# Kernel tuning notes

Measured on AMD Instinct MI355X. Metric: run time of the kernel, lower is better.

Reference implementation:

```python
import jax, jax.numpy as jnp
import numpy as np

B, S, D, H = 2, 2048, 1024, 16
HD = D // H
MASK_VALUE = -1000000.0


def setup_inputs() -> dict:
    key = jax.random.key(0)
    ks = jax.random.split(key, 8)
    scale = 1.0 / np.sqrt(D)
    return {
        "Q": jax.random.normal(ks[0], (B, S, D), jnp.float32),
        "K": jax.random.normal(ks[1], (B, S, D), jnp.float32),
        "V": jax.random.normal(ks[2], (B, S, D), jnp.float32),
        "valid_lens": jax.random.randint(ks[3], (B,), 0, S).astype(jnp.int32),
        "Wq": jax.random.normal(ks[4], (D, D), jnp.float32) * scale,
        "Wk": jax.random.normal(ks[5], (D, D), jnp.float32) * scale,
        "Wv": jax.random.normal(ks[6], (D, D), jnp.float32) * scale,
        "Wo": jax.random.normal(ks[7], (D, D), jnp.float32) * scale,
    }


def _split_heads(x):
    # [B,S,D] -> [B,H,S,HD]
    return x.reshape(B, S, H, HD).transpose(0, 2, 1, 3)


def reference(Q, K, V, valid_lens, Wq, Wk, Wv, Wo):
    q = _split_heads(Q @ Wq)
    k = _split_heads(K @ Wk)
    v = _split_heads(V @ Wv)
    # scores: [B,H,Sq,Sk]
    scores = jnp.einsum("bhqd,bhkd->bhqk", q, k) / jnp.sqrt(jnp.float32(HD))
    # mask key positions >= valid_len (per batch, broadcast over heads/queries)
    key_pos = jnp.arange(S)  # [Sk]
    mask = key_pos[None, None, None, :] < valid_lens[:, None, None, None]
    scores = jnp.where(mask, scores, MASK_VALUE)
    attn = jax.nn.softmax(scores, axis=-1)
    out = jnp.einsum("bhqk,bhkd->bhqd", attn, v)  # [B,H,S,HD]
    out = out.transpose(0, 2, 1, 3).reshape(B, S, D)
    return out @ Wo
```

## Files before the change

### kernel.cpp

```cpp
#include <hip/hip_runtime.h>
#include <stdint.h>

#define B_ 2
#define S_ 2048
#define D_ 1024
#define H_ 16
#define HD_ 64
#define MG_ (B_*S_)
#define MASKV -1000000.0f
#define LP_ 72
#define LO_ 68

typedef __bf16 bf16;
typedef bf16 bf16x8 __attribute__((ext_vector_type(8)));
typedef bf16 bf16x4 __attribute__((ext_vector_type(4)));
typedef float f32x4 __attribute__((ext_vector_type(4)));

#define MFMA(a, b, c) __builtin_amdgcn_mfma_f32_16x16x32_bf16(a, b, c, 0, 0, 0)

__global__ __launch_bounds__(256) void wcast_kernel(const float* __restrict__ W0, const float* __restrict__ W1,
                                                    const float* __restrict__ W2, const float* __restrict__ W3,
                                                    bf16* __restrict__ T) {
  const float* W = blockIdx.z == 0 ? W0 : blockIdx.z == 1 ? W1 : blockIdx.z == 2 ? W2 : W3;
  bf16* Tz = T + (size_t)blockIdx.z * D_ * D_;
  __shared__ float tile[32][33];
  int tx = threadIdx.x & 31, ty = threadIdx.x >> 5;
  int bn = blockIdx.x * 32, bk = blockIdx.y * 32;
#pragma unroll
  for (int i = 0; i < 32; i += 8)
    tile[ty + i][tx] = W[(size_t)(bk + ty + i) * D_ + bn + tx];
  __syncthreads();
#pragma unroll
  for (int i = 0; i < 32; i += 8)
    Tz[(size_t)(bn + ty + i) * D_ + bk + tx] = (bf16)tile[tx][ty + i];
}

__global__ __launch_bounds__(256) void proj_gemm(const float* __restrict__ Qin, const float* __restrict__ Kin,
                                                 const float* __restrict__ Vin, const bf16* __restrict__ WT,
                                                 bf16* __restrict__ qh, bf16* __restrict__ kh,
                                                 bf16* __restrict__ vT) {
  __shared__ alignas(16) bf16 As[128 * 32];
  __shared__ alignas(16) bf16 Bs[128 * 32];
  int mode = blockIdx.z;
  int tid = threadIdx.x, lane = tid & 63, w = tid >> 6;
  int wm = w >> 1, wn = w & 1, ml = lane & 15, quad = lane >> 4;
  int rr = tid >> 3, c4 = (tid & 7) * 4;
  f32x4 acc[4][4] = {};

  if (mode < 2) {
    const float* A = mode ? Kin : Qin;
    const bf16* Bt = WT + (size_t)mode * D_ * D_;
    bf16* dst = mode ? kh : qh;
    float oscale = mode ? 1.0f : 0.125f;
    int m0 = blockIdx.y * 128, n0 = blockIdx.x * 128;
    for (int kk = 0; kk < D_; kk += 32) {
      __syncthreads();
#pragma unroll
      for (int p = 0; p < 4; ++p) {
        float4 v = *(const float4*)&A[(size_t)(m0 + rr + p * 32) * D_ + kk + c4];
        bf16x4 bv; bv[0] = (bf16)v.x; bv[1] = (bf16)v.y; bv[2] = (bf16)v.z; bv[3] = (bf16)v.w;
        *(bf16x4*)&As[(rr + p * 32) * 32 + c4] = bv;
      }
#pragma unroll
      for (int p = 0; p < 2; ++p) {
        int cc = tid + p * 256;
        int nr = cc >> 2, c8 = (cc & 3) * 8;
        *(bf16x8*)&Bs[nr * 32 + c8] = *(const bf16x8*)&Bt[(size_t)(n0 + nr) * D_ + kk + c8];
      }
      __syncthreads();
      bf16x8 af[4], bfr[4];
#pragma unroll
      for (int mt = 0; mt < 4; ++mt) af[mt] = *(bf16x8*)&As[(wm * 64 + mt * 16 + ml) * 32 + quad * 8];
#pragma unroll
      for (int nt = 0; nt < 4; ++nt) bfr[nt] = *(bf16x8*)&Bs[(wn * 64 + nt * 16 + ml) * 32 + quad * 8];
#pragma unroll
      for (int mt = 0; mt < 4; ++mt)
#pragma unroll
        for (int nt = 0; nt < 4; ++nt)
          acc[mt][nt] = MFMA(af[mt], bfr[nt], acc[mt][nt]);
    }
#pragma unroll
    for (int mt = 0; mt < 4; ++mt)
#pragma unroll
      for (int nt = 0; nt < 4; ++nt)
#pragma unroll
        for (int r = 0; r < 4; ++r) {
          int m = m0 + wm * 64 + mt * 16 + quad * 4 + r;
          int n = n0 + wn * 64 + nt * 16 + ml;
          int b = m >> 11, s = m & (S_ - 1), h = n >> 6, hd = n & 63;
          dst[(((size_t)(b * H_ + h)) * S_ + s) * HD_ + hd] = (bf16)(acc[mt][nt][r] * oscale);
        }
  } else {
    const bf16* At = WT + 2ull * D_ * D_;
    int m0 = blockIdx.x * 128;
    int n0 = blockIdx.y * 128;
    for (int kk = 0; kk < D_; kk += 32) {
      __syncthreads();
#pragma unroll
      for (int p = 0; p < 2; ++p) {
        int cc = tid + p * 256;
        int nr = cc >> 2, c8 = (cc & 3) * 8;
        *(bf16x8*)&As[nr * 32 + c8] = *(const bf16x8*)&At[(size_t)(m0 + nr) * D_ + kk + c8];
      }
#pragma unroll
      for (int p = 0; p < 4; ++p) {
        float4 v = *(const float4*)&Vin[(size_t)(n0 + rr + p * 32) * D_ + kk + c4];
        bf16x4 bv; bv[0] = (bf16)v.x; bv[1] = (bf16)v.y; bv[2] = (bf16)v.z; bv[3] = (bf16)v.w;
        *(bf16x4*)&Bs[(rr + p * 32) * 32 + c4] = bv;
      }
      __syncthreads();
      bf16x8 af[4], bfr[4];
#pragma unroll
      for (int mt = 0; mt < 4; ++mt) af[mt] = *(bf16x8*)&As[(wm * 64 + mt * 16 + ml) * 32 + quad * 8];
#pragma unroll
      for (int nt = 0; nt < 4; ++nt) bfr[nt] = *(bf16x8*)&Bs[(wn * 64 + nt * 16 + ml) * 32 + quad * 8];
#pragma unroll
      for (int mt = 0; mt < 4; ++mt)
#pragma unroll
        for (int nt = 0; nt < 4; ++nt)
          acc[mt][nt] = MFMA(af[mt], bfr[nt], acc[mt][nt]);
    }
#pragma unroll
    for (int mt = 0; mt < 4; ++mt)
#pragma unroll
      for (int nt = 0; nt < 4; ++nt)
#pragma unroll
        for (int r = 0; r < 4; ++r) {
          int dcol = m0 + wm * 64 + mt * 16 + quad * 4 + r;
          int n = n0 + wn * 64 + nt * 16 + ml;
          int b = n >> 11, s = n & (S_ - 1), h = dcol >> 6, hd = dcol & 63;
          vT[(((size_t)(b * H_ + h)) * HD_ + hd) * S_ + s] = (bf16)acc[mt][nt][r];
        }
  }
}

__global__ __launch_bounds__(256) void attn_kernel(const bf16* __restrict__ qh, const bf16* __restrict__ kh,
                                                   const bf16* __restrict__ vT, const int* __restrict__ vlen,
                                                   bf16* __restrict__ ctx) {
  __shared__ alignas(16) char ldsraw[35840];
  bf16* Ps = (bf16*)ldsraw;
  float* Om = (float*)ldsraw;
  float* Mv = (float*)(ldsraw + 34816);
  float* Lv = (float*)(ldsraw + 35328);

  int tid = threadIdx.x, lane = tid & 63, w = tid >> 6;
  int ml = lane & 15, quad = lane >> 4;
  int wq = w >> 1, wk = w & 1;
  int bh = blockIdx.y, b = bh >> 4, h = bh & 15;
  int qt = blockIdx.x;
  const bf16* qbase = qh + ((size_t)bh * S_ + qt * 64 + wq * 32) * HD_;
  const bf16* kbase = kh + (size_t)bh * S_ * HD_;
  const bf16* vbase = vT + (size_t)bh * HD_ * S_;
  int valid = vlen[b];
  int nkt = (valid == 0) ? (S_ / 64) : ((valid + 63) >> 6);

  bf16x8 aq[2][2];
#pragma unroll
  for (int mt = 0; mt < 2; ++mt)
#pragma unroll
    for (int half = 0; half < 2; ++half)
      aq[mt][half] = *(const bf16x8*)&qbase[(mt * 16 + ml) * HD_ + half * 32 + quad * 8];

  float m_run[2][4], l_run[2][4];
#pragma unroll
  for (int mt = 0; mt < 2; ++mt)
#pragma unroll
    for (int r = 0; r < 4; ++r) { m_run[mt][r] = -1e30f; l_run[mt][r] = 0.f; }
  f32x4 o[2][4] = {};

  bf16* Pw = Ps + (size_t)w * 32 * LP_;

  for (int kt = wk; kt < nkt; kt += 2) {
    const bf16* kp = kbase + (size_t)kt * 64 * HD_;
    bool tail = (kt * 64 + 64 > valid);
    bf16x8 bk[4][2];
#pragma unroll
    for (int nt = 0; nt < 4; ++nt)
#pragma unroll
      for (int half = 0; half < 2; ++half)
        bk[nt][half] = *(const bf16x8*)&kp[(nt * 16 + ml) * HD_ + half * 32 + quad * 8];

#pragma unroll
    for (int mt = 0; mt < 2; ++mt) {
      f32x4 sc[4];
#pragma unroll
      for (int nt = 0; nt < 4; ++nt) {
        f32x4 c = {};
        c = MFMA(aq[mt][0], bk[nt][0], c);
        c = MFMA(aq[mt][1], bk[nt][1], c);
        sc[nt] = c;
      }
#pragma unroll
      for (int r = 0; r < 4; ++r) {
        float mx = -1e30f;
#pragma unroll
        for (int nt = 0; nt < 4; ++nt) {
          float s = sc[nt][r];
          if (tail) {
            int col = kt * 64 + nt * 16 + ml;
            if (col >= valid) s = MASKV;
          }
          sc[nt][r] = s;
          mx = fmaxf(mx, s);
        }
#pragma unroll
        for (int d = 1; d < 16; d <<= 1) mx = fmaxf(mx, __shfl_xor(mx, d));
        float mnew = fmaxf(m_run[mt][r], mx);
        float ps = 0.f;
#pragma unroll
        for (int nt = 0; nt < 4; ++nt) {
          float p = __expf(sc[nt][r] - mnew);
          sc[nt][r] = p;
          ps += p;
        }
#pragma unroll
        for (int d = 1; d < 16; d <<= 1) ps += __shfl_xor(ps, d);
        float alpha = __expf(m_run[mt][r] - mnew);
        l_run[mt][r] = l_run[mt][r] * alpha + ps;
        m_run[mt][r] = mnew;
#pragma unroll
        for (int ht = 0; ht < 4; ++ht) o[mt][ht][r] *= alpha;
#pragma unroll
        for (int nt = 0; nt < 4; ++nt)
          Pw[(mt * 16 + quad * 4 + r) * LP_ + nt * 16 + ml] = (bf16)sc[nt][r];
      }
    }
#pragma unroll
    for (int ks = 0; ks < 2; ++ks) {
      bf16x8 bv[4];
#pragma unroll
      for (int ht = 0; ht < 4; ++ht)
        bv[ht] = *(const bf16x8*)&vbase[(size_t)(ht * 16 + ml) * S_ + kt * 64 + ks * 32 + quad * 8];
#pragma unroll
      for (int mt = 0; mt < 2; ++mt) {
        bf16x8 ap = *(bf16x8*)&Pw[(mt * 16 + ml) * LP_ + ks * 32 + quad * 8];
#pragma unroll
        for (int ht = 0; ht < 4; ++ht) o[mt][ht] = MFMA(ap, bv[ht], o[mt][ht]);
      }
    }
  }

  __syncthreads();
#pragma unroll
  for (int mt = 0; mt < 2; ++mt) {
#pragma unroll
    for (int r = 0; r < 4; ++r) {
      int rl = mt * 16 + quad * 4 + r;
#pragma unroll
      for (int ht = 0; ht < 4; ++ht)
        Om[(w * 32 + rl) * LO_ + ht * 16 + ml] = o[mt][ht][r];
      if (ml == 0) {
        Mv[w * 32 + rl] = m_run[mt][r];
        Lv[w * 32 + rl] = l_run[mt][r];
      }
    }
  }
  __syncthreads();
#pragma unroll 4
  for (int rr = 0; rr < 16; ++rr) {
    int rg = w * 16 + rr;
    int wqs = rg >> 5, rl = rg & 31;
    int s0 = (wqs * 2) * 32 + rl, s1 = (wqs * 2 + 1) * 32 + rl;
    float ma = Mv[s0], mb = Mv[s1];
    float ms = fmaxf(ma, mb);
    float ca = __expf(ma - ms), cb = __expf(mb - ms);
    float ls = ca * Lv[s0] + cb * Lv[s1];
    float ov = ca * Om[s0 * LO_ + lane] + cb * Om[s1 * LO_ + lane];
    ctx[((size_t)b * S_ + qt * 64 + rg) * D_ + h * 64 + lane] = (bf16)(ov / ls);
  }
}

__global__ __launch_bounds__(256) void out_gemm(const bf16* __restrict__ ctx, const bf16* __restrict__ WoT,
                                                float* __restrict__ out) {
  __shared__ alignas(16) bf16 As[128 * 32];
  __shared__ alignas(16) bf16 Bs[64 * 32];
  int tid = threadIdx.x, lane = tid & 63, w = tid >> 6;
  int wm = w >> 1, wn = w & 1, ml = lane & 15, quad = lane >> 4;
  int m0 = blockIdx.y * 128, n0 = blockIdx.x * 64;
  f32x4 acc[4][2] = {};
  for (int kk = 0; kk < D_; kk += 32) {
    __syncthreads();
    {
#pragma unroll
      for (int p = 0; p < 2; ++p) {
        int cc = tid + p * 256;
        int nr = cc >> 2, c8 = (cc & 3) * 8;
        *(bf16x8*)&As[nr * 32 + c8] = *(const bf16x8*)&ctx[(size_t)(m0 + nr) * D_ + kk + c8];
      }
      int nr = tid >> 2, c8 = (tid & 3) * 8;
      *(bf16x8*)&Bs[nr * 32 + c8] = *(const bf16x8*)&WoT[(size_t)(n0 + nr) * D_ + kk + c8];
    }
    __syncthreads();
    bf16x8 af[4], bfr[2];
#pragma unroll
    for (int mt = 0; mt < 4; ++mt) af[mt] = *(bf16x8*)&As[(wm * 64 + mt * 16 + ml) * 32 + quad * 8];
#pragma unroll
    for (int nt = 0; nt < 2; ++nt) bfr[nt] = *(bf16x8*)&Bs[(wn * 32 + nt * 16 + ml) * 32 + quad * 8];
#pragma unroll
    for (int mt = 0; mt < 4; ++mt)
#pragma unroll
      for (int nt = 0; nt < 2; ++nt)
        acc[mt][nt] = MFMA(af[mt], bfr[nt], acc[mt][nt]);
  }
#pragma unroll
  for (int mt = 0; mt < 4; ++mt)
#pragma unroll
    for (int nt = 0; nt < 2; ++nt)
#pragma unroll
      for (int r = 0; r < 4; ++r) {
        int m = m0 + wm * 64 + mt * 16 + quad * 4 + r;
        int n = n0 + wn * 32 + nt * 16 + ml;
        out[(size_t)m * D_ + n] = acc[mt][nt][r];
      }
}

extern "C" void kernel_launch(void* const* d_in, const int* in_sizes, int n_in,
                              void* d_out, int out_size, void* d_ws, size_t ws_size,
                              hipStream_t stream) {
  const float* Q = (const float*)d_in[0];
  const float* K = (const float*)d_in[1];
  const float* V = (const float*)d_in[2];
  const int* vl = (const int*)d_in[3];
  const float* Wq = (const float*)d_in[4];
  const float* Wk = (const float*)d_in[5];
  const float* Wv = (const float*)d_in[6];
  const float* Wo = (const float*)d_in[7];
  char* ws = (char*)d_ws;
  bf16* WT  = (bf16*)ws;
  bf16* qh  = (bf16*)(ws + 8ull * 1024 * 1024);
  bf16* kh  = (bf16*)(ws + 16ull * 1024 * 1024);
  bf16* vT  = (bf16*)(ws + 24ull * 1024 * 1024);
  bf16* ctx = (bf16*)(ws + 32ull * 1024 * 1024);
  float* out = (float*)d_out;

  wcast_kernel<<<dim3(32, 32, 4), 256, 0, stream>>>(Wq, Wk, Wv, Wo, WT);
  proj_gemm<<<dim3(D_ / 128, MG_ / 128, 3), 256, 0, stream>>>(Q, K, V, WT, qh, kh, vT);
  attn_kernel<<<dim3(S_ / 64, B_ * H_), 256, 0, stream>>>(qh, kh, vT, vl, ctx);
  out_gemm<<<dim3(D_ / 64, MG_ / 128), 256, 0, stream>>>(ctx, WT + 3ull * D_ * D_, out);
}
```

Measured before the change: 243.6 us.

## Use direct global-to-LDS loads for bf16 tiles and remap block order for XCD locality

Replaces the register-staged bf16 weight and ctx tile loads in the projection and output GEMMs with global_load_lds 16-byte direct-to-LDS transfers, which removes VGPR round trips. The projection kernel is unified into a single loop for all three modes by swapping the A/B LDS roles for the V path. All three main kernels now use a 1D grid with a swizzled block index, so that blocks sharing operands (same head, or same row tile) land on one XCD (blockIdx modulo 8) for better L2 reuse. This relies on the LDS layout produced by the direct loads matching the expected row stride, and it adds index arithmetic.

```diff
diff --git a/kernel.cpp b/kernel.cpp
--- a/kernel.cpp
+++ b/kernel.cpp
@@ -18,6 +18,11 @@
 
 #define MFMA(a, b, c) __builtin_amdgcn_mfma_f32_16x16x32_bf16(a, b, c, 0, 0, 0)
 
+__device__ __forceinline__ void gl_lds16(const bf16* g, bf16* l) {
+  __builtin_amdgcn_global_load_lds((const __attribute__((address_space(1))) void*)g,
+                                   (__attribute__((address_space(3))) void*)l, 16, 0, 0);
+}
+
 __global__ __launch_bounds__(256) void wcast_kernel(const float* __restrict__ W0, const float* __restrict__ W1,
                                                     const float* __restrict__ W2, const float* __restrict__ W3,
                                                     bf16* __restrict__ T) {
@@ -39,46 +44,54 @@
                                                  const float* __restrict__ Vin, const bf16* __restrict__ WT,
                                                  bf16* __restrict__ qh, bf16* __restrict__ kh,
                                                  bf16* __restrict__ vT) {
-  __shared__ alignas(16) bf16 As[128 * 32];
-  __shared__ alignas(16) bf16 Bs[128 * 32];
-  int mode = blockIdx.z;
+  __shared__ alignas(16) bf16 Asf[128 * 32];
+  __shared__ alignas(16) bf16 Ash[128 * 32];
+  int mode = blockIdx.y;
+  int bx = blockIdx.x;
+  int i1 = (bx & 7) + ((bx >> 6) << 3);
+  int i2 = (bx >> 3) & 7;
   int tid = threadIdx.x, lane = tid & 63, w = tid >> 6;
   int wm = w >> 1, wn = w & 1, ml = lane & 15, quad = lane >> 4;
   int rr = tid >> 3, c4 = (tid & 7) * 4;
+  int l4 = lane >> 2, k8 = (lane & 3) * 8;
   f32x4 acc[4][4] = {};
 
+  const float* Fp = mode == 0 ? Qin : mode == 1 ? Kin : Vin;
+  const bf16* Hp = WT + (size_t)mode * D_ * D_;
+  int frow0 = i1 * 128, hrow0 = i2 * 128;
+  bf16* Xs = (mode < 2) ? Asf : Ash;
+  bf16* Ys = (mode < 2) ? Ash : Asf;
+
+  for (int kk = 0; kk < D_; kk += 32) {
+    __syncthreads();
+#pragma unroll
+    for (int j = 0; j < 2; ++j) {
+      int chunk = w * 2 + j;
+      gl_lds16(&Hp[(size_t)(hrow0 + chunk * 16 + l4) * D_ + kk + k8], &Ash[chunk * 16 * 32]);
+    }
+#pragma unroll
+    for (int p = 0; p < 4; ++p) {
+      float4 v = *(const float4*)&Fp[(size_t)(frow0 + rr + p * 32) * D_ + kk + c4];
+      bf16x4 bv; bv[0] = (bf16)v.x; bv[1] = (bf16)v.y; bv[2] = (bf16)v.z; bv[3] = (bf16)v.w;
+      *(bf16x4*)&Asf[(rr + p * 32) * 32 + c4] = bv;
+    }
+    __syncthreads();
+    bf16x8 af[4], bfr[4];
+#pragma unroll
+    for (int mt = 0; mt < 4; ++mt) af[mt] = *(bf16x8*)&Xs[(wm * 64 + mt * 16 + ml) * 32 + quad * 8];
+#pragma unroll
+    for (int nt = 0; nt < 4; ++nt) bfr[nt] = *(bf16x8*)&Ys[(wn * 64 + nt * 16 + ml) * 32 + quad * 8];
+#pragma unroll
+    for (int mt = 0; mt < 4; ++mt)
+#pragma unroll
+      for (int nt = 0; nt < 4; ++nt)
+        acc[mt][nt] = MFMA(af[mt], bfr[nt], acc[mt][nt]);
+  }
+
   if (mode < 2) {
-    const float* A = mode ? Kin : Qin;
-    const bf16* Bt = WT + (size_t)mode * D_ * D_;
     bf16* dst = mode ? kh : qh;
     float oscale = mode ? 1.0f : 0.125f;
-    int m0 = blockIdx.y * 128, n0 = blockIdx.x * 128;
-    for (int kk = 0; kk < D_; kk += 32) {
-      __syncthreads();
-#pragma unroll
-      for (int p = 0; p < 4; ++p) {
-        float4 v = *(const float4*)&A[(size_t)(m0 + rr + p * 32) * D_ + kk + c4];
-        bf16x4 bv; bv[0] = (bf16)v.x; bv[1] = (bf16)v.y; bv[2] = (bf16)v.z; bv[3] = (bf16)v.w;
-        *(bf16x4*)&As[(rr + p * 32) * 32 + c4] = bv;
-      }
-#pragma unroll
-      for (int p = 0; p < 2; ++p) {
-        int cc = tid + p * 256;
-        int nr = cc >> 2, c8 = (cc & 3) * 8;
-        *(bf16x8*)&Bs[nr * 32 + c8] = *(const bf16x8*)&Bt[(size_t)(n0 + nr) * D_ + kk + c8];
-      }
-      __syncthreads();
-      bf16x8 af[4], bfr[4];
-#pragma unroll
-      for (int mt = 0; mt < 4; ++mt) af[mt] = *(bf16x8*)&As[(wm * 64 + mt * 16 + ml) * 32 + quad * 8];
-#pragma unroll
-      for (int nt = 0; nt < 4; ++nt) bfr[nt] = *(bf16x8*)&Bs[(wn * 64 + nt * 16 + ml) * 32 + quad * 8];
-#pragma unroll
-      for (int mt = 0; mt < 4; ++mt)
-#pragma unroll
-        for (int nt = 0; nt < 4; ++nt)
-          acc[mt][nt] = MFMA(af[mt], bfr[nt], acc[mt][nt]);
-    }
+    int m0 = i1 * 128, n0 = i2 * 128;
 #pragma unroll
     for (int mt = 0; mt < 4; ++mt)
 #pragma unroll
@@ -91,35 +104,7 @@
           dst[(((size_t)(b * H_ + h)) * S_ + s) * HD_ + hd] = (bf16)(acc[mt][nt][r] * oscale);
         }
   } else {
-    const bf16* At = WT + 2ull * D_ * D_;
-    int m0 = blockIdx.x * 128;
-    int n0 = blockIdx.y * 128;
-    for (int kk = 0; kk < D_; kk += 32) {
-      __syncthreads();
-#pragma unroll
-      for (int p = 0; p < 2; ++p) {
-        int cc = tid + p * 256;
-        int nr = cc >> 2, c8 = (cc & 3) * 8;
-        *(bf16x8*)&As[nr * 32 + c8] = *(const bf16x8*)&At[(size_t)(m0 + nr) * D_ + kk + c8];
-      }
-#pragma unroll
-      for (int p = 0; p < 4; ++p) {
-        float4 v = *(const float4*)&Vin[(size_t)(n0 + rr + p * 32) * D_ + kk + c4];
-        bf16x4 bv; bv[0] = (bf16)v.x; bv[1] = (bf16)v.y; bv[2] = (bf16)v.z; bv[3] = (bf16)v.w;
-        *(bf16x4*)&Bs[(rr + p * 32) * 32 + c4] = bv;
-      }
-      __syncthreads();
-      bf16x8 af[4], bfr[4];
-#pragma unroll
-      for (int mt = 0; mt < 4; ++mt) af[mt] = *(bf16x8*)&As[(wm * 64 + mt * 16 + ml) * 32 + quad * 8];
-#pragma unroll
-      for (int nt = 0; nt < 4; ++nt) bfr[nt] = *(bf16x8*)&Bs[(wn * 64 + nt * 16 + ml) * 32 + quad * 8];
-#pragma unroll
-      for (int mt = 0; mt < 4; ++mt)
-#pragma unroll
-        for (int nt = 0; nt < 4; ++nt)
-          acc[mt][nt] = MFMA(af[mt], bfr[nt], acc[mt][nt]);
-    }
+    int m0 = i2 * 128, n0 = i1 * 128;
 #pragma unroll
     for (int mt = 0; mt < 4; ++mt)
 #pragma unroll
@@ -146,8 +131,10 @@
   int tid = threadIdx.x, lane = tid & 63, w = tid >> 6;
   int ml = lane & 15, quad = lane >> 4;
   int wq = w >> 1, wk = w & 1;
-  int bh = blockIdx.y, b = bh >> 4, h = bh & 15;
-  int qt = blockIdx.x;
+  int bx = blockIdx.x;
+  int bh = (bx & 7) + ((bx >> 8) << 3);
+  int qt = (bx >> 3) & 31;
+  int b = bh >> 4, h = bh & 15;
   const bf16* qbase = qh + ((size_t)bh * S_ + qt * 64 + wq * 32) * HD_;
   const bf16* kbase = kh + (size_t)bh * S_ * HD_;
   const bf16* vbase = vT + (size_t)bh * HD_ * S_;
@@ -274,22 +261,22 @@
                                                 float* __restrict__ out) {
   __shared__ alignas(16) bf16 As[128 * 32];
   __shared__ alignas(16) bf16 Bs[64 * 32];
+  int bx = blockIdx.x;
+  int mt8 = (bx & 7) + ((bx >> 7) << 3);
+  int ntile = (bx >> 3) & 15;
   int tid = threadIdx.x, lane = tid & 63, w = tid >> 6;
   int wm = w >> 1, wn = w & 1, ml = lane & 15, quad = lane >> 4;
-  int m0 = blockIdx.y * 128, n0 = blockIdx.x * 64;
+  int l4 = lane >> 2, k8 = (lane & 3) * 8;
+  int m0 = mt8 * 128, n0 = ntile * 64;
   f32x4 acc[4][2] = {};
   for (int kk = 0; kk < D_; kk += 32) {
     __syncthreads();
-    {
-#pragma unroll
-      for (int p = 0; p < 2; ++p) {
-        int cc = tid + p * 256;
-        int nr = cc >> 2, c8 = (cc & 3) * 8;
-        *(bf16x8*)&As[nr * 32 + c8] = *(const bf16x8*)&ctx[(size_t)(m0 + nr) * D_ + kk + c8];
-      }
-      int nr = tid >> 2, c8 = (tid & 3) * 8;
-      *(bf16x8*)&Bs[nr * 32 + c8] = *(const bf16x8*)&WoT[(size_t)(n0 + nr) * D_ + kk + c8];
-    }
+#pragma unroll
+    for (int j = 0; j < 2; ++j) {
+      int chunk = w * 2 + j;
+      gl_lds16(&ctx[(size_t)(m0 + chunk * 16 + l4) * D_ + kk + k8], &As[chunk * 16 * 32]);
+    }
+    gl_lds16(&WoT[(size_t)(n0 + w * 16 + l4) * D_ + kk + k8], &Bs[w * 16 * 32]);
     __syncthreads();
     bf16x8 af[4], bfr[2];
 #pragma unroll
@@ -334,7 +321,7 @@
   float* out = (float*)d_out;
 
   wcast_kernel<<<dim3(32, 32, 4), 256, 0, stream>>>(Wq, Wk, Wv, Wo, WT);
-  proj_gemm<<<dim3(D_ / 128, MG_ / 128, 3), 256, 0, stream>>>(Q, K, V, WT, qh, kh, vT);
-  attn_kernel<<<dim3(S_ / 64, B_ * H_), 256, 0, stream>>>(qh, kh, vT, vl, ctx);
-  out_gemm<<<dim3(D_ / 64, MG_ / 128), 256, 0, stream>>>(ctx, WT + 3ull * D_ * D_, out);
-}
+  proj_gemm<<<dim3(256, 3), 256, 0, stream>>>(Q, K, V, WT, qh, kh, vT);
+  attn_kernel<<<dim3(1024), 256, 0, stream>>>(qh, kh, vT, vl, ctx);
+  out_gemm<<<dim3(512), 256, 0, stream>>>(ctx, WT + 3ull * D_ * D_, out);
+}
```

New measurement: 237.4 us. 2.5% less time.
